# Kernel tuning notes

Measured on AMD Instinct MI355X. Metric: run time of the kernel, lower is better.

## Reference

```python
import jax, jax.numpy as jnp
import numpy as np

B, CIN, COUT, K, H, W, NPTS = 8, 256, 256, 4, 128, 128, 512


def setup_inputs() -> dict:
    key = jax.random.key(0)
    ks = jax.random.split(key, 9)
    inp = {
        'input': jax.random.normal(ks[0], (B, CIN, H, W), dtype=jnp.float32),
        'ax': jax.random.uniform(ks[1], (B, NPTS), dtype=jnp.float32) * (W - 1),
        'ay': jax.random.uniform(ks[2], (B, NPTS), dtype=jnp.float32) * (H - 1),
        # 1x1 conv = matmul over channels
        'Wp': jax.random.normal(ks[3], (COUT, CIN), dtype=jnp.float32) * 0.02,
        'bp': jnp.zeros((COUT,), dtype=jnp.float32),
        'Woff': jax.random.normal(ks[4], (K, 2, CIN), dtype=jnp.float32) * 0.02,
        'boff': jnp.zeros((K, 2), dtype=jnp.float32),
        'Ww': jax.random.normal(ks[5], (K, CIN), dtype=jnp.float32) * 0.02,
        'bw': jnp.zeros((K,), dtype=jnp.float32),
    }
    return inp


def _bilinear_zeros(img, xs, ys):
    """grid_sample(mode='bilinear', padding_mode='zeros').
    img: [b, C, H, W]; xs, ys: [b, H, W] source pixel coords. Returns [b, H, W, C]."""
    b, C, h, w = img.shape
    img_hwc = jnp.transpose(img, (0, 2, 3, 1))  # [b, H, W, C]
    x0 = jnp.floor(xs)
    y0 = jnp.floor(ys)
    wx1 = xs - x0
    wy1 = ys - y0
    bidx = jnp.arange(b)[:, None, None]

    def corner(xi, yi, wgt):
        valid = (xi >= 0) & (xi < w) & (yi >= 0) & (yi < h)
        xc = jnp.clip(xi, 0, w - 1).astype(jnp.int32)
        yc = jnp.clip(yi, 0, h - 1).astype(jnp.int32)
        v = img_hwc[bidx, yc, xc]  # [b, H, W, C]
        return v * (jnp.where(valid, wgt, 0.0))[..., None]

    out = (corner(x0, y0, (1 - wx1) * (1 - wy1))
           + corner(x0 + 1, y0, wx1 * (1 - wy1))
           + corner(x0, y0 + 1, (1 - wx1) * wy1)
           + corner(x0 + 1, y0 + 1, wx1 * wy1))
    return out


def _forward(input, ax, ay, Wp, bp, Woff, boff, Ww, bw):
    b, c, h, w = input.shape
    k = Ww.shape[0]
    proj = jnp.einsum('bchw,oc->bohw', input, Wp) + bp[None, :, None, None]
    # k flow fields [k, b, 2, h, w]
    flows = jnp.einsum('bchw,koc->kbohw', input, Woff) + boff[:, None, :, None, None]
    logits = jnp.einsum('bchw,kc->bkhw', input, Ww) + bw[None, :, None, None]
    wts = jax.nn.softmax(logits, axis=1)  # [b, k, h, w]

    gx = jnp.arange(w, dtype=input.dtype)[None, None, :]
    gy = jnp.arange(h, dtype=input.dtype)[None, :, None]
    # torch normalization: n = 2*v/(dim-1)-1, then grid_sample(align_corners=False)
    # maps n -> ((n+1)*dim - 1)/2 = v*dim/(dim-1) - 0.5
    sx_scale = w / max(w - 1, 1)
    sy_scale = h / max(h - 1, 1)

    # gather sum_k wts_k * sampled_k at every pixel (loop over small fixed k)
    summed = jnp.zeros((b, h, w, proj.shape[1]), dtype=input.dtype)
    for i in range(k):
        sx = (gx + flows[i, :, 0]) * sx_scale - 0.5  # [b, h, w]
        sy = (gy + flows[i, :, 1]) * sy_scale - 0.5
        summed = summed + wts[:, i, :, :, None] * _bilinear_zeros(proj, sx, sy)

    # point gather: feat[num, :, id[1], id[0]] with id = trunc((ax, ay))
    ix = jnp.trunc(ax).astype(jnp.int32)  # width index
    iy = jnp.trunc(ay).astype(jnp.int32)  # height index
    out = summed[jnp.arange(b)[:, None], iy, ix]  # [b, num_pts, out_ch]
    return out


def reference(input, ax, ay, Wp, bp, Woff, boff, Ww, bw):
    return _forward(input, ax, ay, Wp, bp, Woff, boff, Ww, bw)
```

## Files before the change

### kernel.cpp

```cpp
#include <hip/hip_runtime.h>
#include <hip/hip_fp16.h>

#define B_      8
#define CIN_    256
#define COUT_   256
#define K_      4
#define H_      128
#define W_      128
#define NPTS_   512

#define NPTS_TOT_   (B_ * NPTS_)
#define T_BYTES_    ((size_t)B_ * H_ * W_ * CIN_ * sizeof(__half))
#define WTS_OFF_    T_BYTES_
#define SITES_OFF_  (WTS_OFF_   + (size_t)NPTS_TOT_ * 16 * 4)
#define WSUM_OFF_   (SITES_OFF_ + (size_t)NPTS_TOT_ * 16 * 4)
#define WS_NEED_    (WSUM_OFF_  + (size_t)NPTS_TOT_ * 4)

__global__ __launch_bounds__(256) void ka_kernel(
    const float* __restrict__ input,
    const float* __restrict__ ax,
    const float* __restrict__ ay,
    const float* __restrict__ Woff,
    const float* __restrict__ boff,
    const float* __restrict__ Ww,
    const float* __restrict__ bw,
    __half* __restrict__ T,
    float* __restrict__ wts_g,
    int*   __restrict__ sites_g,
    float* __restrict__ wsums_g)
{
    __shared__ float lt[32][129];
    __shared__ float xs[CIN_];
    __shared__ float dotv[12];
    __shared__ float wc16[16];

    const int bid = blockIdx.x;
    const int t   = threadIdx.x;

    if (bid < 8192) {
        const int b   = bid >> 10;
        const int r   = bid & 1023;
        const int h   = r >> 3;
        const int c0  = (r & 7) << 5;

        const int c = t >> 3;
        const int m = t & 7;
        const float* __restrict__ src = input + (((size_t)(b * CIN_ + c0 + c) * H_ + h) * W_);
        #pragma unroll
        for (int q = 0; q < 4; ++q) {
            const int w = m * 4 + q * 32;
            const float4 v = *reinterpret_cast<const float4*>(src + w);
            lt[c][w]     = v.x;
            lt[c][w + 1] = v.y;
            lt[c][w + 2] = v.z;
            lt[c][w + 3] = v.w;
        }
        __syncthreads();

        const int w  = t >> 1;
        const int hc = (t & 1) << 4;
        unsigned int words[8];
        #pragma unroll
        for (int i = 0; i < 8; ++i) {
            __half2 h2 = __floats2half2_rn(lt[hc + 2 * i][w], lt[hc + 2 * i + 1][w]);
            words[i] = *reinterpret_cast<unsigned int*>(&h2);
        }
        __half* dst = T + (((size_t)(b * H_ + h) * W_ + w) * CIN_ + c0 + hc);
        reinterpret_cast<uint4*>(dst)[0] = make_uint4(words[0], words[1], words[2], words[3]);
        reinterpret_cast<uint4*>(dst)[1] = make_uint4(words[4], words[5], words[6], words[7]);
        return;
    }

    const int pt = bid - 8192;
    const int b  = pt >> 9;

    const int ix = (int)truncf(ax[pt]);
    const int iy = (int)truncf(ay[pt]);
    const float* __restrict__ chan = input + (size_t)b * (CIN_ * H_ * W_) + (size_t)t * (H_ * W_);

    xs[t] = chan[iy * W_ + ix];
    __syncthreads();

    const int wave = t >> 6;
    const int lane = t & 63;
    #pragma unroll
    for (int r = 0; r < 3; ++r) {
        const int d = wave * 3 + r;
        const float* __restrict__ row = (d < 8) ? (Woff + d * CIN_) : (Ww + (d - 8) * CIN_);
        float s = 0.f;
        #pragma unroll
        for (int q = 0; q < 4; ++q) {
            const int c = lane + q * 64;
            s = fmaf(xs[c], row[c], s);
        }
        #pragma unroll
        for (int off = 32; off > 0; off >>= 1)
            s += __shfl_down(s, off);
        if (lane == 0) dotv[d] = s;
    }
    __syncthreads();

    if (t < 4) {
        const int k = t;
        const float l0 = dotv[8]  + bw[0];
        const float l1 = dotv[9]  + bw[1];
        const float l2 = dotv[10] + bw[2];
        const float l3 = dotv[11] + bw[3];
        const float mx = fmaxf(fmaxf(l0, l1), fmaxf(l2, l3));
        const float e0 = expf(l0 - mx), e1 = expf(l1 - mx);
        const float e2 = expf(l2 - mx), e3 = expf(l3 - mx);
        const float ek = (k == 0) ? e0 : (k == 1) ? e1 : (k == 2) ? e2 : e3;
        const float wk = ek / (e0 + e1 + e2 + e3);

        const float scale = 128.0f / 127.0f;
        const float fx = dotv[2 * k]     + boff[2 * k];
        const float fy = dotv[2 * k + 1] + boff[2 * k + 1];
        const float sxv = ((float)ix + fx) * scale - 0.5f;
        const float syv = ((float)iy + fy) * scale - 0.5f;
        const float x0f = floorf(sxv), y0f = floorf(syv);
        const float wx1 = sxv - x0f, wy1 = syv - y0f;
        const int x0 = (int)x0f, y0 = (int)y0f;
        #pragma unroll
        for (int ci = 0; ci < 4; ++ci) {
            const int xi = x0 + (ci & 1);
            const int yi = y0 + (ci >> 1);
            const bool valid = (xi >= 0) & (xi < W_) & (yi >= 0) & (yi < H_);
            float wc = ((ci & 1) ? wx1 : 1.f - wx1) * ((ci >> 1) ? wy1 : 1.f - wy1) * wk;
            wc = valid ? wc : 0.f;
            const int xc = min(max(xi, 0), W_ - 1);
            const int yc = min(max(yi, 0), H_ - 1);
            const int idx = k * 4 + ci;
            wc16[idx] = wc;
            wts_g[pt * 16 + idx]   = wc;
            sites_g[pt * 16 + idx] = ((b * H_ + yc) * W_ + xc) * CIN_;
        }
    }
    __syncthreads();
    if (t == 0) {
        float s = 0.f;
        #pragma unroll
        for (int i = 0; i < 16; ++i) s += wc16[i];
        wsums_g[pt] = s;
    }
}

__global__ __launch_bounds__(512) void kb_kernel(
    const __half* __restrict__ T,
    const float* __restrict__ Wp,
    const float* __restrict__ bp,
    const float* __restrict__ wts_g,
    const int*   __restrict__ sites_g,
    const float* __restrict__ wsums_g,
    float* __restrict__ out)
{
    __shared__ float xsh[16][260];
    __shared__ float wtile[32 * 256];
    __shared__ float swts[16][16];
    __shared__ int   ssites[16][16];
    __shared__ float swsum[16];

    const int blk = blockIdx.x;
    const int p0g = blk << 4;
    const int tid = threadIdx.x;

    if (tid < 256) {
        swts[tid >> 4][tid & 15]   = wts_g[p0g * 16 + tid];
        ssites[tid >> 4][tid & 15] = sites_g[p0g * 16 + tid];
    } else if (tid < 256 + 16) {
        swsum[tid - 256] = wsums_g[p0g + (tid - 256)];
    }
    __syncthreads();

    {
        const int p   = tid >> 5;
        const int oct = tid & 31;
        const int c0  = oct << 3;
        float a[8] = {0.f, 0.f, 0.f, 0.f, 0.f, 0.f, 0.f, 0.f};
        #pragma unroll
        for (int s = 0; s < 16; ++s) {
            const float w = swts[p][s];
            const uint4 raw = *reinterpret_cast<const uint4*>(T + (size_t)ssites[p][s] + c0);
            const __half* hh = reinterpret_cast<const __half*>(&raw);
            #pragma unroll
            for (int j = 0; j < 8; ++j)
                a[j] = fmaf(w, __half2float(hh[j]), a[j]);
        }
        *reinterpret_cast<float4*>(&xsh[p][c0])     = make_float4(a[0], a[1], a[2], a[3]);
        *reinterpret_cast<float4*>(&xsh[p][c0 + 4]) = make_float4(a[4], a[5], a[6], a[7]);
    }
    __syncthreads();

    const int oq = tid & 63;
    const int pp = tid >> 6;
    const int o0 = oq << 2;
    const int p0 = pp << 1;

    const float4 bpv = *reinterpret_cast<const float4*>(bp + o0);
    const float ws0 = swsum[p0], ws1 = swsum[p0 + 1];
    float a00 = bpv.x * ws0, a01 = bpv.y * ws0, a02 = bpv.z * ws0, a03 = bpv.w * ws0;
    float a10 = bpv.x * ws1, a11 = bpv.y * ws1, a12 = bpv.z * ws1, a13 = bpv.w * ws1;

    for (int ch = 0; ch < 8; ++ch) {
        #pragma unroll
        for (int r = 0; r < 4; ++r) {
            const int idx = r * 512 + tid;
            const int c4  = idx & 7;
            const int o   = idx >> 3;
            const float4 v = *reinterpret_cast<const float4*>(Wp + (size_t)o * CIN_ + ch * 32 + c4 * 4);
            const float vv[4] = {v.x, v.y, v.z, v.w};
            #pragma unroll
            for (int m = 0; m < 4; ++m) {
                const int c  = c4 * 4 + m;
                const int os = (o >> 2) ^ (c & 7);
                wtile[c * 256 + (os << 2) + (o & 3)] = vv[m];
            }
        }
        __syncthreads();

        const int cb = ch * 32;
        #pragma unroll
        for (int cq = 0; cq < 8; ++cq) {
            const float4 x0 = *reinterpret_cast<const float4*>(&xsh[p0][cb + (cq << 2)]);
            const float4 x1 = *reinterpret_cast<const float4*>(&xsh[p0 + 1][cb + (cq << 2)]);
            const float x0a[4] = {x0.x, x0.y, x0.z, x0.w};
            const float x1a[4] = {x1.x, x1.y, x1.z, x1.w};
            #pragma unroll
            for (int m = 0; m < 4; ++m) {
                const int c = (cq << 2) + m;
                const float4 wv = *reinterpret_cast<const float4*>(
                    &wtile[c * 256 + ((oq ^ (c & 7)) << 2)]);
                const float xm0 = x0a[m], xm1 = x1a[m];
                a00 = fmaf(xm0, wv.x, a00); a01 = fmaf(xm0, wv.y, a01);
                a02 = fmaf(xm0, wv.z, a02); a03 = fmaf(xm0, wv.w, a03);
                a10 = fmaf(xm1, wv.x, a10); a11 = fmaf(xm1, wv.y, a11);
                a12 = fmaf(xm1, wv.z, a12); a13 = fmaf(xm1, wv.w, a13);
            }
        }
        __syncthreads();
    }

    float* o_row0 = out + (size_t)(p0g + p0) * COUT_ + o0;
    float* o_row1 = out + (size_t)(p0g + p0 + 1) * COUT_ + o0;
    *reinterpret_cast<float4*>(o_row0) = make_float4(a00, a01, a02, a03);
    *reinterpret_cast<float4*>(o_row1) = make_float4(a10, a11, a12, a13);
}

__global__ __launch_bounds__(256) void ple_point_kernel(
    const float* __restrict__ input, const float* __restrict__ ax,
    const float* __restrict__ ay, const float* __restrict__ Wp,
    const float* __restrict__ bp, const float* __restrict__ Woff,
    const float* __restrict__ boff, const float* __restrict__ Ww,
    const float* __restrict__ bw, float* __restrict__ out)
{
    const int gid = blockIdx.x;
    const int b   = gid >> 9;
    const int tid = threadIdx.x;

    __shared__ float xs[CIN_];
    __shared__ float dotv[12];

    const int ix = (int)truncf(ax[gid]);
    const int iy = (int)truncf(ay[gid]);
    const float* __restrict__ chan = input + (size_t)b * (CIN_ * H_ * W_) + (size_t)tid * (H_ * W_);

    xs[tid] = chan[iy * W_ + ix];
    __syncthreads();

    const int wave = tid >> 6;
    const int lane = tid & 63;
    #pragma unroll
    for (int r = 0; r < 3; ++r) {
        const int d = wave * 3 + r;
        const float* __restrict__ row = (d < 8) ? (Woff + d * CIN_) : (Ww + (d - 8) * CIN_);
        float s = 0.f;
        #pragma unroll
        for (int q = 0; q < 4; ++q) s = fmaf(xs[lane + q * 64], row[lane + q * 64], s);
        #pragma unroll
        for (int off = 32; off > 0; off >>= 1) s += __shfl_down(s, off);
        if (lane == 0) dotv[d] = s;
    }
    __syncthreads();

    float lg[K_];
    float mx = -1e30f;
    #pragma unroll
    for (int k = 0; k < K_; ++k) { lg[k] = dotv[8 + k] + bw[k]; mx = fmaxf(mx, lg[k]); }
    float se = 0.f;
    #pragma unroll
    for (int k = 0; k < K_; ++k) { lg[k] = expf(lg[k] - mx); se += lg[k]; }
    const float inv_se = 1.f / se;
    const float scale = 128.0f / 127.0f;

    float xacc = 0.f, wsum = 0.f;
    #pragma unroll
    for (int k = 0; k < K_; ++k) {
        const float wk = lg[k] * inv_se;
        const float fx = dotv[2 * k] + boff[2 * k];
        const float fy = dotv[2 * k + 1] + boff[2 * k + 1];
        const float sxv = ((float)ix + fx) * scale - 0.5f;
        const float syv = ((float)iy + fy) * scale - 0.5f;
        const float x0f = floorf(sxv), y0f = floorf(syv);
        const float wx1 = sxv - x0f, wy1 = syv - y0f;
        const int x0 = (int)x0f, y0 = (int)y0f;
        const int x1 = x0 + 1, y1 = y0 + 1;
        const float w00 = (1.f - wx1) * (1.f - wy1) * wk;
        const float w10 = wx1 * (1.f - wy1) * wk;
        const float w01 = (1.f - wx1) * wy1 * wk;
        const float w11 = wx1 * wy1 * wk;
        const bool vx0 = (x0 >= 0) && (x0 < W_);
        const bool vx1 = (x1 >= 0) && (x1 < W_);
        if (y0 >= 0 && y0 < H_) {
            const float* rowp = chan + y0 * W_;
            if (vx0) { xacc = fmaf(w00, rowp[x0], xacc); wsum += w00; }
            if (vx1) { xacc = fmaf(w10, rowp[x1], xacc); wsum += w10; }
        }
        if (y1 >= 0 && y1 < H_) {
            const float* rowp = chan + y1 * W_;
            if (vx0) { xacc = fmaf(w01, rowp[x0], xacc); wsum += w01; }
            if (vx1) { xacc = fmaf(w11, rowp[x1], xacc); wsum += w11; }
        }
    }

    xs[tid] = xacc;
    __syncthreads();

    const float* __restrict__ wrow = Wp + tid * CIN_;
    float a0 = bp[tid] * wsum, a1 = 0.f, a2 = 0.f, a3 = 0.f;
    #pragma unroll 4
    for (int c = 0; c < CIN_; c += 4) {
        const float4 wv = *reinterpret_cast<const float4*>(wrow + c);
        a0 = fmaf(wv.x, xs[c], a0);
        a1 = fmaf(wv.y, xs[c + 1], a1);
        a2 = fmaf(wv.z, xs[c + 2], a2);
        a3 = fmaf(wv.w, xs[c + 3], a3);
    }
    out[(size_t)gid * COUT_ + tid] = (a0 + a1) + (a2 + a3);
}

extern "C" void kernel_launch(void* const* d_in, const int* in_sizes, int n_in,
                              void* d_out, int out_size, void* d_ws, size_t ws_size,
                              hipStream_t stream) {
    const float* input = (const float*)d_in[0];
    const float* ax    = (const float*)d_in[1];
    const float* ay    = (const float*)d_in[2];
    const float* Wp    = (const float*)d_in[3];
    const float* bp    = (const float*)d_in[4];
    const float* Woff  = (const float*)d_in[5];
    const float* boff  = (const float*)d_in[6];
    const float* Ww    = (const float*)d_in[7];
    const float* bw    = (const float*)d_in[8];
    float* out = (float*)d_out;

    if (ws_size >= WS_NEED_) {
        __half* T      = (__half*)d_ws;
        float*  wts_g  = (float*)((char*)d_ws + WTS_OFF_);
        int*    sites_g= (int*)  ((char*)d_ws + SITES_OFF_);
        float*  wsums_g= (float*)((char*)d_ws + WSUM_OFF_);

        ka_kernel<<<dim3(8192 + NPTS_TOT_), dim3(256), 0, stream>>>(
            input, ax, ay, Woff, boff, Ww, bw, T, wts_g, sites_g, wsums_g);
        kb_kernel<<<dim3(256), dim3(512), 0, stream>>>(
            T, Wp, bp, wts_g, sites_g, wsums_g, out);
    } else {
        ple_point_kernel<<<dim3(B_ * NPTS_), dim3(256), 0, stream>>>(
            input, ax, ay, Wp, bp, Woff, boff, Ww, bw, out);
    }
}
```

Measured before the change: 73.04 us.

## Move per-point offset computation into gather kernel and restructure transpose

The per-point flow and softmax weight computation moves from the transpose kernel into the gather/projection kernel. It now reads the point's channel column from the fp16 transposed tensor instead of scattered fp32 input, which removes the workspace round trip for weights and sites. The transpose kernel is rewritten to handle two rows and 64 channels per block, staging half2-packed data through LDS so each thread writes 128 contiguous bytes. The offset and softmax logits are now computed from fp16-rounded inputs, which slightly changes numerics.

```diff
diff --git a/kernel.cpp b/kernel.cpp
--- a/kernel.cpp
+++ b/kernel.cpp
@@ -11,101 +11,131 @@
 
 #define NPTS_TOT_   (B_ * NPTS_)
 #define T_BYTES_    ((size_t)B_ * H_ * W_ * CIN_ * sizeof(__half))
-#define WTS_OFF_    T_BYTES_
-#define SITES_OFF_  (WTS_OFF_   + (size_t)NPTS_TOT_ * 16 * 4)
-#define WSUM_OFF_   (SITES_OFF_ + (size_t)NPTS_TOT_ * 16 * 4)
-#define WS_NEED_    (WSUM_OFF_  + (size_t)NPTS_TOT_ * 4)
 
 __global__ __launch_bounds__(256) void ka_kernel(
     const float* __restrict__ input,
+    __half* __restrict__ T)
+{
+    __shared__ unsigned int lt[32][256];
+
+    const int bid = blockIdx.x;
+    const int b   = bid >> 8;
+    const int r   = bid & 255;
+    const int cg  = r >> 6;
+    const int hh  = r & 63;
+
+    const int t    = threadIdx.x;
+    const int wv   = t >> 6;
+    const int lane = t & 63;
+
+    const size_t base = ((size_t)(b * CIN_ + cg * 64) * H_ + 2 * hh) * W_;
+    float4 A[8], Bv[8];
+    #pragma unroll
+    for (int ii = 0; ii < 8; ++ii) {
+        const int c = wv * 16 + 2 * ii;
+        const float* rowA = input + base + (size_t)c * (H_ * W_);
+        const float* rowB = rowA + (H_ * W_);
+        A[ii]  = *reinterpret_cast<const float4*>(rowA + lane * 4);
+        Bv[ii] = *reinterpret_cast<const float4*>(rowB + lane * 4);
+    }
+    #pragma unroll
+    for (int ii = 0; ii < 8; ++ii) {
+        const int i = wv * 8 + ii;
+        __half2 h0 = __floats2half2_rn(A[ii].x, Bv[ii].x);
+        __half2 h1 = __floats2half2_rn(A[ii].y, Bv[ii].y);
+        __half2 h2 = __floats2half2_rn(A[ii].z, Bv[ii].z);
+        __half2 h3 = __floats2half2_rn(A[ii].w, Bv[ii].w);
+        const unsigned int w0 = *reinterpret_cast<unsigned int*>(&h0);
+        const unsigned int w1 = *reinterpret_cast<unsigned int*>(&h1);
+        const unsigned int w2 = *reinterpret_cast<unsigned int*>(&h2);
+        const unsigned int w3 = *reinterpret_cast<unsigned int*>(&h3);
+        *reinterpret_cast<uint4*>(&lt[i][lane * 4]) = make_uint4(w0, w1, w2, w3);
+    }
+    __syncthreads();
+
+    unsigned int wreg[32];
+    #pragma unroll
+    for (int i = 0; i < 32; ++i) wreg[i] = lt[i][t];
+
+    const int h = 2 * hh + (t >> 7);
+    const int w = t & 127;
+    __half* dst = T + ((size_t)(b * H_ + h) * W_ + w) * CIN_ + cg * 64;
+    uint4* d4 = reinterpret_cast<uint4*>(dst);
+    #pragma unroll
+    for (int j = 0; j < 8; ++j)
+        d4[j] = make_uint4(wreg[4 * j], wreg[4 * j + 1], wreg[4 * j + 2], wreg[4 * j + 3]);
+}
+
+__global__ __launch_bounds__(512) void kb_kernel(
+    const __half* __restrict__ T,
     const float* __restrict__ ax,
     const float* __restrict__ ay,
+    const float* __restrict__ Wp,
+    const float* __restrict__ bp,
     const float* __restrict__ Woff,
     const float* __restrict__ boff,
     const float* __restrict__ Ww,
     const float* __restrict__ bw,
-    __half* __restrict__ T,
-    float* __restrict__ wts_g,
-    int*   __restrict__ sites_g,
-    float* __restrict__ wsums_g)
+    float* __restrict__ out)
 {
-    __shared__ float lt[32][129];
-    __shared__ float xs[CIN_];
-    __shared__ float dotv[12];
-    __shared__ float wc16[16];
-
-    const int bid = blockIdx.x;
-    const int t   = threadIdx.x;
-
-    if (bid < 8192) {
-        const int b   = bid >> 10;
-        const int r   = bid & 1023;
-        const int h   = r >> 3;
-        const int c0  = (r & 7) << 5;
-
-        const int c = t >> 3;
-        const int m = t & 7;
-        const float* __restrict__ src = input + (((size_t)(b * CIN_ + c0 + c) * H_ + h) * W_);
-        #pragma unroll
-        for (int q = 0; q < 4; ++q) {
-            const int w = m * 4 + q * 32;
-            const float4 v = *reinterpret_cast<const float4*>(src + w);
-            lt[c][w]     = v.x;
-            lt[c][w + 1] = v.y;
-            lt[c][w + 2] = v.z;
-            lt[c][w + 3] = v.w;
-        }
-        __syncthreads();
-
-        const int w  = t >> 1;
-        const int hc = (t & 1) << 4;
-        unsigned int words[8];
-        #pragma unroll
-        for (int i = 0; i < 8; ++i) {
-            __half2 h2 = __floats2half2_rn(lt[hc + 2 * i][w], lt[hc + 2 * i + 1][w]);
-            words[i] = *reinterpret_cast<unsigned int*>(&h2);
-        }
-        __half* dst = T + (((size_t)(b * H_ + h) * W_ + w) * CIN_ + c0 + hc);
-        reinterpret_cast<uint4*>(dst)[0] = make_uint4(words[0], words[1], words[2], words[3]);
-        reinterpret_cast<uint4*>(dst)[1] = make_uint4(words[4], words[5], words[6], words[7]);
-        return;
-    }
-
-    const int pt = bid - 8192;
-    const int b  = pt >> 9;
-
-    const int ix = (int)truncf(ax[pt]);
-    const int iy = (int)truncf(ay[pt]);
-    const float* __restrict__ chan = input + (size_t)b * (CIN_ * H_ * W_) + (size_t)t * (H_ * W_);
-
-    xs[t] = chan[iy * W_ + ix];
-    __syncthreads();
-
-    const int wave = t >> 6;
-    const int lane = t & 63;
-    #pragma unroll
-    for (int r = 0; r < 3; ++r) {
-        const int d = wave * 3 + r;
+    __shared__ float xcol[16][264];
+    __shared__ float xsh[16][260];
+    __shared__ float wtile[32 * 256];
+    __shared__ float dotv[16][12];
+    __shared__ float swts[16][16];
+    __shared__ int   ssites[16][16];
+    __shared__ float swsum[16];
+    __shared__ int   spix[16], spiy[16];
+
+    const int blk = blockIdx.x;
+    const int p0g = blk << 4;
+    const int b   = p0g >> 9;
+    const int tid = threadIdx.x;
+
+    if (tid < 16) {
+        const int gid = p0g + tid;
+        spix[tid] = (int)truncf(ax[gid]);
+        spiy[tid] = (int)truncf(ay[gid]);
+    }
+    __syncthreads();
+
+    {
+        const int p  = tid >> 5;
+        const int c8 = (tid & 31) << 3;
+        const size_t px = (size_t)(b * H_ + spiy[p]) * W_ + spix[p];
+        const uint4 raw = *reinterpret_cast<const uint4*>(T + px * CIN_ + c8);
+        const __half* hv = reinterpret_cast<const __half*>(&raw);
+        #pragma unroll
+        for (int j = 0; j < 8; ++j) xcol[p][c8 + j] = __half2float(hv[j]);
+    }
+    __syncthreads();
+
+    const int wv   = tid >> 6;
+    const int lane = tid & 63;
+    for (int r = 0; r < 24; ++r) {
+        const int idx = wv * 24 + r;
+        const int p = idx / 12;
+        const int d = idx % 12;
         const float* __restrict__ row = (d < 8) ? (Woff + d * CIN_) : (Ww + (d - 8) * CIN_);
         float s = 0.f;
         #pragma unroll
         for (int q = 0; q < 4; ++q) {
             const int c = lane + q * 64;
-            s = fmaf(xs[c], row[c], s);
+            s = fmaf(xcol[p][c], row[c], s);
         }
         #pragma unroll
         for (int off = 32; off > 0; off >>= 1)
             s += __shfl_down(s, off);
-        if (lane == 0) dotv[d] = s;
-    }
-    __syncthreads();
-
-    if (t < 4) {
-        const int k = t;
-        const float l0 = dotv[8]  + bw[0];
-        const float l1 = dotv[9]  + bw[1];
-        const float l2 = dotv[10] + bw[2];
-        const float l3 = dotv[11] + bw[3];
+        if (lane == 0) dotv[p][d] = s;
+    }
+    __syncthreads();
+
+    if (tid < 64) {
+        const int p = tid >> 2, k = tid & 3;
+        const float l0 = dotv[p][8]  + bw[0];
+        const float l1 = dotv[p][9]  + bw[1];
+        const float l2 = dotv[p][10] + bw[2];
+        const float l3 = dotv[p][11] + bw[3];
         const float mx = fmaxf(fmaxf(l0, l1), fmaxf(l2, l3));
         const float e0 = expf(l0 - mx), e1 = expf(l1 - mx);
         const float e2 = expf(l2 - mx), e3 = expf(l3 - mx);
@@ -113,10 +143,10 @@
         const float wk = ek / (e0 + e1 + e2 + e3);
 
         const float scale = 128.0f / 127.0f;
-        const float fx = dotv[2 * k]     + boff[2 * k];
-        const float fy = dotv[2 * k + 1] + boff[2 * k + 1];
-        const float sxv = ((float)ix + fx) * scale - 0.5f;
-        const float syv = ((float)iy + fy) * scale - 0.5f;
+        const float fx = dotv[p][2 * k]     + boff[2 * k];
+        const float fy = dotv[p][2 * k + 1] + boff[2 * k + 1];
+        const float sxv = ((float)spix[p] + fx) * scale - 0.5f;
+        const float syv = ((float)spiy[p] + fy) * scale - 0.5f;
         const float x0f = floorf(sxv), y0f = floorf(syv);
         const float wx1 = sxv - x0f, wy1 = syv - y0f;
         const int x0 = (int)x0f, y0 = (int)y0f;
@@ -129,47 +159,18 @@
             wc = valid ? wc : 0.f;
             const int xc = min(max(xi, 0), W_ - 1);
             const int yc = min(max(yi, 0), H_ - 1);
-            const int idx = k * 4 + ci;
-            wc16[idx] = wc;
-            wts_g[pt * 16 + idx]   = wc;
-            sites_g[pt * 16 + idx] = ((b * H_ + yc) * W_ + xc) * CIN_;
-        }
-    }
-    __syncthreads();
-    if (t == 0) {
+            swts[p][k * 4 + ci]   = wc;
+            ssites[p][k * 4 + ci] = ((b * H_ + yc) * W_ + xc) * CIN_;
+        }
+    }
+    __syncthreads();
+
+    if (tid < 16) {
         float s = 0.f;
         #pragma unroll
-        for (int i = 0; i < 16; ++i) s += wc16[i];
-        wsums_g[pt] = s;
-    }
-}
-
-__global__ __launch_bounds__(512) void kb_kernel(
-    const __half* __restrict__ T,
-    const float* __restrict__ Wp,
-    const float* __restrict__ bp,
-    const float* __restrict__ wts_g,
-    const int*   __restrict__ sites_g,
-    const float* __restrict__ wsums_g,
-    float* __restrict__ out)
-{
-    __shared__ float xsh[16][260];
-    __shared__ float wtile[32 * 256];
-    __shared__ float swts[16][16];
-    __shared__ int   ssites[16][16];
-    __shared__ float swsum[16];
-
-    const int blk = blockIdx.x;
-    const int p0g = blk << 4;
-    const int tid = threadIdx.x;
-
-    if (tid < 256) {
-        swts[tid >> 4][tid & 15]   = wts_g[p0g * 16 + tid];
-        ssites[tid >> 4][tid & 15] = sites_g[p0g * 16 + tid];
-    } else if (tid < 256 + 16) {
-        swsum[tid - 256] = wsums_g[p0g + (tid - 256)];
-    }
-    __syncthreads();
+        for (int i = 0; i < 16; ++i) s += swts[tid][i];
+        swsum[tid] = s;
+    }
 
     {
         const int p   = tid >> 5;
@@ -180,10 +181,10 @@
         for (int s = 0; s < 16; ++s) {
             const float w = swts[p][s];
             const uint4 raw = *reinterpret_cast<const uint4*>(T + (size_t)ssites[p][s] + c0);
-            const __half* hh = reinterpret_cast<const __half*>(&raw);
+            const __half* hv = reinterpret_cast<const __half*>(&raw);
             #pragma unroll
             for (int j = 0; j < 8; ++j)
-                a[j] = fmaf(w, __half2float(hh[j]), a[j]);
+                a[j] = fmaf(w, __half2float(hv[j]), a[j]);
         }
         *reinterpret_cast<float4*>(&xsh[p][c0])     = make_float4(a[0], a[1], a[2], a[3]);
         *reinterpret_cast<float4*>(&xsh[p][c0 + 4]) = make_float4(a[4], a[5], a[6], a[7]);
@@ -227,13 +228,13 @@
             #pragma unroll
             for (int m = 0; m < 4; ++m) {
                 const int c = (cq << 2) + m;
-                const float4 wv = *reinterpret_cast<const float4*>(
+                const float4 wvv = *reinterpret_cast<const float4*>(
                     &wtile[c * 256 + ((oq ^ (c & 7)) << 2)]);
                 const float xm0 = x0a[m], xm1 = x1a[m];
-                a00 = fmaf(xm0, wv.x, a00); a01 = fmaf(xm0, wv.y, a01);
-                a02 = fmaf(xm0, wv.z, a02); a03 = fmaf(xm0, wv.w, a03);
-                a10 = fmaf(xm1, wv.x, a10); a11 = fmaf(xm1, wv.y, a11);
-                a12 = fmaf(xm1, wv.z, a12); a13 = fmaf(xm1, wv.w, a13);
+                a00 = fmaf(xm0, wvv.x, a00); a01 = fmaf(xm0, wvv.y, a01);
+                a02 = fmaf(xm0, wvv.z, a02); a03 = fmaf(xm0, wvv.w, a03);
+                a10 = fmaf(xm1, wvv.x, a10); a11 = fmaf(xm1, wvv.y, a11);
+                a12 = fmaf(xm1, wvv.z, a12); a13 = fmaf(xm1, wvv.w, a13);
             }
         }
         __syncthreads();
@@ -328,11 +329,11 @@
     float a0 = bp[tid] * wsum, a1 = 0.f, a2 = 0.f, a3 = 0.f;
     #pragma unroll 4
     for (int c = 0; c < CIN_; c += 4) {
-        const float4 wv = *reinterpret_cast<const float4*>(wrow + c);
-        a0 = fmaf(wv.x, xs[c], a0);
-        a1 = fmaf(wv.y, xs[c + 1], a1);
-        a2 = fmaf(wv.z, xs[c + 2], a2);
-        a3 = fmaf(wv.w, xs[c + 3], a3);
+        const float4 wvv = *reinterpret_cast<const float4*>(wrow + c);
+        a0 = fmaf(wvv.x, xs[c], a0);
+        a1 = fmaf(wvv.y, xs[c + 1], a1);
+        a2 = fmaf(wvv.z, xs[c + 2], a2);
+        a3 = fmaf(wvv.w, xs[c + 3], a3);
     }
     out[(size_t)gid * COUT_ + tid] = (a0 + a1) + (a2 + a3);
 }
@@ -351,16 +352,11 @@
     const float* bw    = (const float*)d_in[8];
     float* out = (float*)d_out;
 
-    if (ws_size >= WS_NEED_) {
-        __half* T      = (__half*)d_ws;
-        float*  wts_g  = (float*)((char*)d_ws + WTS_OFF_);
-        int*    sites_g= (int*)  ((char*)d_ws + SITES_OFF_);
-        float*  wsums_g= (float*)((char*)d_ws + WSUM_OFF_);
-
-        ka_kernel<<<dim3(8192 + NPTS_TOT_), dim3(256), 0, stream>>>(
-            input, ax, ay, Woff, boff, Ww, bw, T, wts_g, sites_g, wsums_g);
-        kb_kernel<<<dim3(256), dim3(512), 0, stream>>>(
-            T, Wp, bp, wts_g, sites_g, wsums_g, out);
+    if (ws_size >= T_BYTES_) {
+        __half* T = (__half*)d_ws;
+        ka_kernel<<<dim3(B_ * 4 * (H_ / 2)), dim3(256), 0, stream>>>(input, T);
+        kb_kernel<<<dim3(NPTS_TOT_ / 16), dim3(512), 0, stream>>>(
+            T, ax, ay, Wp, bp, Woff, boff, Ww, bw, out);
     } else {
         ple_point_kernel<<<dim3(B_ * NPTS_), dim3(256), 0, stream>>>(
             input, ax, ay, Wp, bp, Woff, boff, Ww, bw, out);
```

After: 75.47 us. +3.3%, slower.
